# Optimization experiments

Measured on AMD Instinct MI355X. Metric: run time of the kernel, lower is better.

Reference implementation:

```python
import jax, jax.numpy as jnp
import numpy as np

H = 256  # GRU hidden size


def _gru_scan(state, lengths, Wih, Whh, bih, bhh):
    # state: [B, T, D]; run a batched GRU over time, freezing h once t >= lengths[b]
    B, T, D = state.shape
    # precompute input gates for all timesteps: [T, B, 3H]
    gi_all = jnp.einsum('btd,gd->tbg', state, Wih) + bih

    def step(h, inp):
        gi, t = inp
        gh = h @ Whh.T + bhh                       # [B, 3H]
        i_r, i_z, i_n = jnp.split(gi, 3, axis=-1)
        h_r, h_z, h_n = jnp.split(gh, 3, axis=-1)
        r = jax.nn.sigmoid(i_r + h_r)
        z = jax.nn.sigmoid(i_z + h_z)
        n = jnp.tanh(i_n + r * h_n)
        h_new = (1.0 - z) * n + z * h              # torch GRUCell update
        mask = (t < lengths)[:, None]              # ragged: stop updating past length
        return jnp.where(mask, h_new, h), None

    h0 = jnp.zeros((B, H), state.dtype)
    h, _ = jax.lax.scan(step, h0, (gi_all, jnp.arange(T)))
    return h  # [B, H] = hidden after lengths[b] GRU steps


def _mlp(x, w1, b1, w2, b2, w3, b3, w4, b4, wq, bq):
    x = jax.nn.relu(x @ w1.T + b1)
    x = jax.nn.relu(x @ w2.T + b2)
    x = jax.nn.relu(x @ w3.T + b3)
    x = jax.nn.relu(x @ w4.T + b4)
    return x @ wq.T + bq  # [B, 1]


def setup_inputs() -> dict:
    key = jax.random.key(0)
    ks = jax.random.split(key, 40)
    B, T, D, A = 2048, 64, 15, 1
    inp = {}
    inp['state'] = jax.random.normal(ks[0], (B, T, D), jnp.float32)
    inp['action'] = jax.random.normal(ks[1], (B, A), jnp.float32)
    inp['lengths'] = jax.random.randint(ks[2], (B,), 1, T + 1, jnp.int32)
    i = 3
    for t in (1, 2):
        for name, shape, fan in [('Wih', (3 * H, D), D), ('Whh', (3 * H, H), H),
                                 ('bih', (3 * H,), H), ('bhh', (3 * H,), H)]:
            inp[f'g{t}_{name}'] = jax.random.normal(ks[i], shape, jnp.float32) / np.sqrt(fan)
            i += 1
        for name, (o, n) in [('fc1', (1024, H + D + A)), ('fc2', (1024, 1024)),
                             ('fc3', (512, 1024)), ('fc4', (256, 512)), ('q', (1, 256))]:
            inp[f'{name}_{t}_w'] = jax.random.normal(ks[i], (o, n), jnp.float32) / np.sqrt(n)
            i += 1
            inp[f'{name}_{t}_b'] = jax.random.normal(ks[i], (o,), jnp.float32) * 0.01
            i += 1
    return inp


def reference(state, action, lengths,
              g1_Wih, g1_Whh, g1_bih, g1_bhh,
              fc1_1_w, fc1_1_b, fc2_1_w, fc2_1_b, fc3_1_w, fc3_1_b,
              fc4_1_w, fc4_1_b, q_1_w, q_1_b,
              g2_Wih, g2_Whh, g2_bih, g2_bhh,
              fc1_2_w, fc1_2_b, fc2_2_w, fc2_2_b, fc3_2_w, fc3_2_b,
              fc4_2_w, fc4_2_b, q_2_w, q_2_b):
    h1 = _gru_scan(state, lengths, g1_Wih, g1_Whh, g1_bih, g1_bhh)
    h2 = _gru_scan(state, lengths, g2_Wih, g2_Whh, g2_bih, g2_bhh)
    aug = jnp.concatenate([state[:, 0, :], action], axis=-1)  # [B, 16]
    x1 = jnp.concatenate([aug, h1], axis=-1)                  # [B, 272]
    x2 = jnp.concatenate([aug, h2], axis=-1)
    out1 = _mlp(x1, fc1_1_w, fc1_1_b, fc2_1_w, fc2_1_b, fc3_1_w, fc3_1_b,
                fc4_1_w, fc4_1_b, q_1_w, q_1_b)
    out2 = _mlp(x2, fc1_2_w, fc1_2_b, fc2_2_w, fc2_2_b, fc3_2_w, fc3_2_b,
                fc4_2_w, fc4_2_b, q_2_w, q_2_b)
    return (out1, out2)
```

## Files before the change

kernel.cpp:

```cpp
#include <hip/hip_runtime.h>

typedef float  f32x4 __attribute__((ext_vector_type(4)));
typedef short  s16x8 __attribute__((ext_vector_type(8)));
typedef __bf16 b16x8 __attribute__((ext_vector_type(8)));

#define DEV __device__ __forceinline__

DEV unsigned short f2b(float f) {
  unsigned u = __builtin_bit_cast(unsigned, f);
  u = (u + 0x7FFFu + ((u >> 16) & 1u)) >> 16;
  return (unsigned short)u;
}
DEV b16x8 ld8(const unsigned short* p) {
  return __builtin_bit_cast(b16x8, *(const s16x8*)p);
}
DEV float sigm(float x) { return __builtin_amdgcn_rcpf(1.f + __expf(-x)); }
DEV float tanh_fast(float x) {
  float e = __expf(2.f * x);
  return 1.f - 2.f * __builtin_amdgcn_rcpf(e + 1.f);
}
DEV void async16(const unsigned short* g, unsigned short* l) {
  __builtin_amdgcn_global_load_lds(
      (const __attribute__((address_space(1))) unsigned int*)g,
      (__attribute__((address_space(3))) unsigned int*)l, 16, 0, 0);
}
DEV f32x4 mfma_bf16(b16x8 a, b16x8 b, f32x4 c) {
  return __builtin_amdgcn_mfma_f32_16x16x32_bf16(a, b, c, 0, 0, 0);
}

struct PrepArgs {
  const float *whh[2], *wih[2], *bih[2], *bhh[2];
  const float *src[2][4];
  unsigned short *waug[2], *dst[2][4];
  const float *qb[2];
  float *out;
};

__global__ __launch_bounds__(256) void prep_kernel(PrepArgs p) {
  const int job = blockIdx.y;
  const int i0 = blockIdx.x * 256 + threadIdx.x;
  const int stride = gridDim.x * 256;
  if (job < 2) {
    const float* whh = p.whh[job];
    const float* wih = p.wih[job];
    const float* bih = p.bih[job];
    const float* bhh = p.bhh[job];
    unsigned short* dst = p.waug[job];
    for (int idx = i0; idx < 768 * 288; idx += stride) {
      int j = idx / 288, k = idx - j * 288;
      float v = 0.f;
      if (k < 256) {
        int o = k & 31;
        int kk = (k & 0x1E0) + (o >> 1) + ((o & 1) << 4);
        v = whh[j * 256 + kk];
      } else if (k < 271)  v = wih[j * 15 + (k - 256)];
      else if (k == 271)   v = (j < 512) ? (bih[j] + bhh[j]) : bih[j];
      dst[idx] = f2b(v);
    }
  } else if (job < 10) {
    const int jj = job - 2, br = jj >> 2, ly = jj & 3;
    const int rowsA[4] = {1024, 1024, 512, 256};
    const int scA[4]   = {272, 1024, 1024, 512};
    const int dcA[4]   = {288, 1024, 1024, 512};
    const float* src = p.src[br][ly];
    unsigned short* dst = p.dst[br][ly];
    const int sc = scA[ly], dc = dcA[ly], tot = rowsA[ly] * dc;
    for (int idx = i0; idx < tot; idx += stride) {
      int r = idx / dc, c = idx - r * dc;
      float v = (c < sc) ? src[r * sc + c] : 0.f;
      dst[idx] = f2b(v);
    }
  } else {
    for (int idx = i0; idx < 4096; idx += stride)
      p.out[idx] = p.qb[idx >> 11][0];
  }
}

#define GRU_LDS_BYTES 98432
__attribute__((amdgpu_waves_per_eu(2, 2)))
__global__ void __launch_bounds__(512) gru_kernel(
    const float* __restrict__ state, const float* __restrict__ action,
    const int* __restrict__ lengths,
    const unsigned short* __restrict__ waug0, const unsigned short* __restrict__ waug1,
    const float* __restrict__ bhh0, const float* __restrict__ bhh1,
    unsigned short* __restrict__ x0, unsigned short* __restrict__ x1) {
  extern __shared__ char smem[];
  unsigned short* W7   = (unsigned short*)smem;
  unsigned short* SgL  = (unsigned short*)(smem + 49152);
  unsigned*       Hb2  = (unsigned*)(smem + 81920);
  int* lenS = (int*)(smem + 98304);
  int* mlS  = (int*)(smem + 98368);

  const int tid = threadIdx.x;
  const int lane = tid & 63, w = tid >> 6;
  const int l15 = lane & 15, q = lane >> 4;
  const int g = blockIdx.x & 1;
  const int r0 = (blockIdx.x >> 1) * 16;

  const unsigned short* Waug = g ? waug1 : waug0;
  const float* bhh = g ? bhh1 : bhh0;
  unsigned short* xout = g ? x1 : x0;

  for (int i = tid; i < 4096; i += 512) Hb2[i] = 0;
  if (tid < 16) lenS[tid] = lengths[r0 + tid];
  for (int s = tid; s < 64 * 32; s += 512) {
    const int t = s >> 5, L = s & 31;
    const int q2 = L >> 4, r = L & 15;
    const float* sp = state + (size_t)(r0 + r) * 960 + t * 15;
    s16x8 h;
#pragma unroll
    for (int j = 0; j < 8; j++) {
      const int k = q2 * 8 + j;
      float v = (k < 15) ? sp[k] : (k == 15 ? 1.0f : 0.f);
      h[j] = (short)f2b(v);
    }
    *(s16x8*)(SgL + (size_t)s * 8) = h;
  }
  __syncthreads();
  if (tid == 0) {
    int m = 1;
    for (int i = 0; i < 16; i++) m = lenS[i] > m ? lenS[i] : m;
    *mlS = m;
  }

  int c0[6];
  c0[0] = 32 * w;       c0[1] = 32 * w + 16;
  c0[2] = 256 + 32 * w; c0[3] = 256 + 32 * w + 16;
  c0[4] = 512 + 32 * w; c0[5] = 512 + 32 * w + 16;

  b16x8 wres[6][7];
  b16x8 waugf[6];
#pragma unroll
  for (int i = 0; i < 6; i++) {
    const unsigned short* bpi = Waug + (size_t)(c0[i] + l15) * 288 + q * 8;
#pragma unroll
    for (int j = 0; j < 7; j++) wres[i][j] = ld8(bpi + j * 32);
    waugf[i] = ld8(bpi + 256);
    *(s16x8*)(W7 + (size_t)i * 4096 + tid * 8) =
        __builtin_bit_cast(s16x8, ld8(bpi + 7 * 32));
  }
  float bnH[2] = {bhh[c0[4] + l15], bhh[c0[5] + l15]};
  int len4[4];
#pragma unroll
  for (int r = 0; r < 4; r++) len4[r] = lenS[q * 4 + r];

  int aOff[8];
#pragma unroll
  for (int j = 0; j < 8; j++) {
    const int cj = 4 * j + q;
    const int pj = (cj & 24) | ((cj & 7) ^ (l15 & 7));
    aOff[j] = l15 * 128 + pj * 4;
  }
  int wOff[4];
#pragma unroll
  for (int rg = 0; rg < 4; rg++) {
    const int row = q * 4 + rg;
    const int cb = 4 * w + (l15 >> 2);
    const int pw = (cb & 24) | ((cb & 7) ^ (row & 7));
    wOff[rg] = row * 128 + pw * 4 + (l15 & 3);
  }
  __syncthreads();
  const int maxlen = *mlS;

  float hold[2][4] = {{0, 0, 0, 0}, {0, 0, 0, 0}};
  int poff = 0;

  for (int t = 0; t < maxlen; ++t) {
    __syncthreads();

    f32x4 acc[6];
#pragma unroll
    for (int i = 0; i < 6; i++) acc[i] = f32x4{0.f, 0.f, 0.f, 0.f};

    {
      b16x8 a8 = ld8(SgL + t * 256 + ((q & 1) * 16 + l15) * 8);
#pragma unroll
      for (int i = 0; i < 6; i++) acc[i] = mfma_bf16(a8, waugf[i], acc[i]);
    }
    f32x4 giN0 = acc[4], giN1 = acc[5];
    acc[4] = acc[4] + bnH[0];
    acc[5] = acc[5] + bnH[1];

    const unsigned* hb = Hb2 + poff;
#pragma unroll
    for (int j = 0; j < 7; j++) {
      b16x8 a = __builtin_bit_cast(b16x8, *(const uint4*)(hb + aOff[j]));
#pragma unroll
      for (int i = 0; i < 6; i++) acc[i] = mfma_bf16(a, wres[i][j], acc[i]);
    }
    {
      b16x8 a = __builtin_bit_cast(b16x8, *(const uint4*)(hb + aOff[7]));
#pragma unroll
      for (int i = 0; i < 6; i++) {
        b16x8 bw = ld8(W7 + (size_t)i * 4096 + tid * 8);
        acc[i] = mfma_bf16(a, bw, acc[i]);
      }
    }

    unsigned* hbw = Hb2 + (poff ^ 2048);
#pragma unroll
    for (int rg = 0; rg < 4; rg++) {
      const bool live = (t < len4[rg]);
      float r0g = sigm(acc[0][rg]);
      float z0 = sigm(acc[2][rg]);
      float n0 = tanh_fast(giN0[rg] + r0g * (acc[4][rg] - giN0[rg]));
      float h0 = n0 + z0 * (hold[0][rg] - n0);
      h0 = live ? h0 : hold[0][rg];
      hold[0][rg] = h0;
      float r1g = sigm(acc[1][rg]);
      float z1 = sigm(acc[3][rg]);
      float n1 = tanh_fast(giN1[rg] + r1g * (acc[5][rg] - giN1[rg]));
      float h1 = n1 + z1 * (hold[1][rg] - n1);
      h1 = live ? h1 : hold[1][rg];
      hold[1][rg] = h1;
      hbw[wOff[rg]] = (unsigned)f2b(h0) | ((unsigned)f2b(h1) << 16);
    }
    poff ^= 2048;
  }

#pragma unroll
  for (int i = 0; i < 2; i++) {
    const int c = 32 * w + 16 * i + l15;
#pragma unroll
    for (int rg = 0; rg < 4; rg++) {
      const int row = q * 4 + rg;
      xout[(size_t)(r0 + row) * 288 + 16 + c] = f2b(hold[i][rg]);
    }
  }
  {
    const int row = tid >> 5, cc = tid & 31;
    float v; int col;
    if (cc < 15)       { v = state[(size_t)(r0 + row) * 960 + cc]; col = cc; }
    else if (cc == 15) { v = action[r0 + row]; col = 15; }
    else               { v = 0.f; col = 256 + cc; }
    xout[(size_t)(r0 + row) * 288 + col] = f2b(v);
  }
}

template <int BM, int BN>
__global__ __launch_bounds__(256, 2) void gemm_bias_relu(
    const unsigned short* __restrict__ A0, const unsigned short* __restrict__ A1,
    const unsigned short* __restrict__ W0, const unsigned short* __restrict__ W1,
    const float* __restrict__ b0, const float* __restrict__ b1,
    unsigned short* __restrict__ Y0, unsigned short* __restrict__ Y1,
    int N, int K) {
  const unsigned short* A = blockIdx.z ? A1 : A0;
  const unsigned short* W = blockIdx.z ? W1 : W0;
  const float* bias = blockIdx.z ? b1 : b0;
  unsigned short* Y = blockIdx.z ? Y1 : Y0;

  constexpr int MT = BM / 32;
  constexpr int NT = BN / 32;
  const int tid = threadIdx.x;
  const int lane = tid & 63, wid = tid >> 6;
  const int wm = wid >> 1, wn = wid & 1;
  const int l15 = lane & 15, q = lane >> 4;
  const int m0 = blockIdx.x * BM, n0 = blockIdx.y * BN;

  __shared__ unsigned short As[BM * 32];
  __shared__ unsigned short Bs[BN * 32];

  f32x4 acc[MT][NT];
#pragma unroll
  for (int mi = 0; mi < MT; mi++)
#pragma unroll
    for (int ni = 0; ni < NT; ni++) acc[mi][ni] = f32x4{0.f, 0.f, 0.f, 0.f};

  const int srow = tid >> 2, scol = (tid & 3) * 8;

  for (int k0 = 0; k0 < K; k0 += 32) {
#pragma unroll
    for (int g64 = 0; g64 < BM / 64; g64++)
      async16(A + (size_t)(m0 + g64 * 64 + srow) * K + scol + k0,
              &As[g64 * 2048 + tid * 8]);
#pragma unroll
    for (int g64 = 0; g64 < BN / 64; g64++)
      async16(W + (size_t)(n0 + g64 * 64 + srow) * K + scol + k0,
              &Bs[g64 * 2048 + tid * 8]);
    __syncthreads();

    b16x8 af[MT], bf[NT];
#pragma unroll
    for (int mi = 0; mi < MT; mi++)
      af[mi] = ld8(&As[(wm * (BM / 2) + mi * 16 + l15) * 32 + q * 8]);
#pragma unroll
    for (int ni = 0; ni < NT; ni++)
      bf[ni] = ld8(&Bs[(wn * (BN / 2) + ni * 16 + l15) * 32 + q * 8]);
#pragma unroll
    for (int mi = 0; mi < MT; mi++)
#pragma unroll
      for (int ni = 0; ni < NT; ni++)
        acc[mi][ni] = mfma_bf16(af[mi], bf[ni], acc[mi][ni]);
    __syncthreads();
  }

#pragma unroll
  for (int ni = 0; ni < NT; ni++) {
    const int col = n0 + wn * (BN / 2) + ni * 16 + l15;
    const float bv = bias[col];
#pragma unroll
    for (int mi = 0; mi < MT; mi++) {
      const int rbase = m0 + wm * (BM / 2) + mi * 16 + q * 4;
#pragma unroll
      for (int rg = 0; rg < 4; rg++) {
        float v = acc[mi][ni][rg] + bv;
        v = fmaxf(v, 0.f);
        Y[(size_t)(rbase + rg) * N + col] = f2b(v);
      }
    }
  }
}

__global__ __launch_bounds__(256, 2) void fc4q_kernel(
    const unsigned short* __restrict__ A0, const unsigned short* __restrict__ A1,
    const unsigned short* __restrict__ W0, const unsigned short* __restrict__ W1,
    const float* __restrict__ b0, const float* __restrict__ b1,
    const float* __restrict__ qw0, const float* __restrict__ qw1,
    float* __restrict__ out) {
  const unsigned short* A = blockIdx.z ? A1 : A0;
  const unsigned short* W = blockIdx.z ? W1 : W0;
  const float* bias = blockIdx.z ? b1 : b0;
  const float* qw = blockIdx.z ? qw1 : qw0;

  const int tid = threadIdx.x;
  const int lane = tid & 63, wn = tid >> 6;
  const int l15 = lane & 15, q = lane >> 4;
  const int m0 = blockIdx.x * 32;
  const int nbase = blockIdx.y * 128;
  const int K = 512;

  __shared__ unsigned short As[32 * 32];
  __shared__ unsigned short Bs[128 * 32];
  __shared__ float red[32][4];

  f32x4 acc[2][2];
#pragma unroll
  for (int mi = 0; mi < 2; mi++)
#pragma unroll
    for (int ni = 0; ni < 2; ni++) acc[mi][ni] = f32x4{0.f, 0.f, 0.f, 0.f};

  const int srow = tid >> 2, scol = (tid & 3) * 8;
  for (int k0 = 0; k0 < K; k0 += 32) {
    if (tid < 128)
      async16(A + (size_t)(m0 + srow) * K + scol + k0, &As[tid * 8]);
#pragma unroll
    for (int g64 = 0; g64 < 2; g64++)
      async16(W + (size_t)(nbase + g64 * 64 + srow) * K + scol + k0,
              &Bs[g64 * 2048 + tid * 8]);
    __syncthreads();

    b16x8 af[2], bf[2];
#pragma unroll
    for (int mi = 0; mi < 2; mi++)
      af[mi] = ld8(&As[(mi * 16 + l15) * 32 + q * 8]);
#pragma unroll
    for (int ni = 0; ni < 2; ni++)
      bf[ni] = ld8(&Bs[(wn * 32 + ni * 16 + l15) * 32 + q * 8]);
#pragma unroll
    for (int mi = 0; mi < 2; mi++)
#pragma unroll
      for (int ni = 0; ni < 2; ni++)
        acc[mi][ni] = mfma_bf16(af[mi], bf[ni], acc[mi][ni]);
    __syncthreads();
  }

#pragma unroll
  for (int mi = 0; mi < 2; mi++) {
#pragma unroll
    for (int rg = 0; rg < 4; rg++) {
      float s = 0.f;
#pragma unroll
      for (int ni = 0; ni < 2; ni++) {
        const int col = nbase + wn * 32 + ni * 16 + l15;
        float v = fmaxf(acc[mi][ni][rg] + bias[col], 0.f);
        s += v * qw[col];
      }
#pragma unroll
      for (int off = 1; off < 16; off <<= 1) s += __shfl_xor(s, off);
      if (l15 == 0) red[mi * 16 + q * 4 + rg][wn] = s;
    }
  }
  __syncthreads();
  if (tid < 32) {
    float t = red[tid][0] + red[tid][1] + red[tid][2] + red[tid][3];
    atomicAdd(out + (size_t)blockIdx.z * 2048 + m0 + tid, t);
  }
}

extern "C" void kernel_launch(void* const* d_in, const int* in_sizes, int n_in,
                              void* d_out, int out_size, void* d_ws, size_t ws_size,
                              hipStream_t stream) {
  const float* state   = (const float*)d_in[0];
  const float* action  = (const float*)d_in[1];
  const int*   lengths = (const int*)d_in[2];
  const float* g_wih[2] = {(const float*)d_in[3], (const float*)d_in[17]};
  const float* g_whh[2] = {(const float*)d_in[4], (const float*)d_in[18]};
  const float* g_bih[2] = {(const float*)d_in[5], (const float*)d_in[19]};
  const float* g_bhh[2] = {(const float*)d_in[6], (const float*)d_in[20]};
  const float* fcw[2][4] = {
      {(const float*)d_in[7], (const float*)d_in[9], (const float*)d_in[11], (const float*)d_in[13]},
      {(const float*)d_in[21], (const float*)d_in[23], (const float*)d_in[25], (const float*)d_in[27]}};
  const float* fcb[2][4] = {
      {(const float*)d_in[8], (const float*)d_in[10], (const float*)d_in[12], (const float*)d_in[14]},
      {(const float*)d_in[22], (const float*)d_in[24], (const float*)d_in[26], (const float*)d_in[28]}};
  const float* qw[2] = {(const float*)d_in[15], (const float*)d_in[29]};
  const float* qb[2] = {(const float*)d_in[16], (const float*)d_in[30]};
  float* out = (float*)d_out;

  uintptr_t base = (uintptr_t)d_ws;
  auto alloc = [&](size_t bytes) -> unsigned short* {
    void* p = (void*)base;
    base += (bytes + 255) & ~(size_t)255;
    return (unsigned short*)p;
  };
  unsigned short *waug[2], *w1b[2], *w2b[2], *w3b[2], *w4b[2], *xb[2], *yA[2], *yB[2];
  for (int g = 0; g < 2; g++) waug[g] = alloc(768 * 288 * 2);
  for (int g = 0; g < 2; g++) w1b[g] = alloc(1024 * 288 * 2);
  for (int g = 0; g < 2; g++) w2b[g] = alloc(1024 * 1024 * 2);
  for (int g = 0; g < 2; g++) w3b[g] = alloc(512 * 1024 * 2);
  for (int g = 0; g < 2; g++) w4b[g] = alloc(256 * 512 * 2);
  for (int g = 0; g < 2; g++) xb[g] = alloc(2048 * 288 * 2);
  for (int g = 0; g < 2; g++) yA[g] = alloc(2048 * 1024 * 2);
  for (int g = 0; g < 2; g++) yB[g] = alloc(2048 * 1024 * 2);
  (void)ws_size; (void)in_sizes; (void)n_in; (void)out_size;

  PrepArgs pa;
  for (int g = 0; g < 2; g++) {
    pa.whh[g] = g_whh[g]; pa.wih[g] = g_wih[g];
    pa.bih[g] = g_bih[g]; pa.bhh[g] = g_bhh[g];
    pa.waug[g] = waug[g];
    pa.src[g][0] = fcw[g][0]; pa.dst[g][0] = w1b[g];
    pa.src[g][1] = fcw[g][1]; pa.dst[g][1] = w2b[g];
    pa.src[g][2] = fcw[g][2]; pa.dst[g][2] = w3b[g];
    pa.src[g][3] = fcw[g][3]; pa.dst[g][3] = w4b[g];
    pa.qb[g] = qb[g];
  }
  pa.out = out;
  prep_kernel<<<dim3(64, 11), 256, 0, stream>>>(pa);

  (void)hipFuncSetAttribute((const void*)gru_kernel,
                            hipFuncAttributeMaxDynamicSharedMemorySize,
                            GRU_LDS_BYTES);
  gru_kernel<<<dim3(256), dim3(512), GRU_LDS_BYTES, stream>>>(
      state, action, lengths, waug[0], waug[1], g_bhh[0], g_bhh[1], xb[0], xb[1]);

  gemm_bias_relu<64, 128><<<dim3(32, 8, 2), 256, 0, stream>>>(
      xb[0], xb[1], w1b[0], w1b[1], fcb[0][0], fcb[1][0], yA[0], yA[1], 1024, 288);
  gemm_bias_relu<64, 128><<<dim3(32, 8, 2), 256, 0, stream>>>(
      yA[0], yA[1], w2b[0], w2b[1], fcb[0][1], fcb[1][1], yB[0], yB[1], 1024, 1024);
  gemm_bias_relu<64, 64><<<dim3(32, 8, 2), 256, 0, stream>>>(
      yB[0], yB[1], w3b[0], w3b[1], fcb[0][2], fcb[1][2], yA[0], yA[1], 512, 1024);
  fc4q_kernel<<<dim3(64, 2, 2), 256, 0, stream>>>(
      yA[0], yA[1], w4b[0], w4b[1], fcb[0][3], fcb[1][3], qw[0], qw[1], out);
}
```

Baseline: 356.7 us.

## Halve GRU block to 4 waves with 64 columns each; retune MLP GEMM tiles

The GRU recurrence kernel now runs 256 threads instead of 512. Each wave owns 64 hidden columns across all three gates, which doubles the per-wave MFMA work and register-resident weights. The input-projection weights move from registers to LDS, raising the LDS footprint to about 147 KB. The goal is to cut per-step barrier cost and cross-wave sync in the serial time loop, at the price of fewer waves to hide latency and heavy register pressure. Separately, fc1/fc2 use 64x64 tiles with twice as many blocks, and the GEMM launch bounds allow 4 blocks per CU.

```diff
diff --git a/kernel.cpp b/kernel.cpp
--- a/kernel.cpp
+++ b/kernel.cpp
@@ -76,9 +76,9 @@
   }
 }
 
-#define GRU_LDS_BYTES 98432
-__attribute__((amdgpu_waves_per_eu(2, 2)))
-__global__ void __launch_bounds__(512) gru_kernel(
+#define GRU_LDS_BYTES 147584
+__attribute__((amdgpu_waves_per_eu(1, 1)))
+__global__ void __launch_bounds__(256) gru_kernel(
     const float* __restrict__ state, const float* __restrict__ action,
     const int* __restrict__ lengths,
     const unsigned short* __restrict__ waug0, const unsigned short* __restrict__ waug1,
@@ -86,10 +86,11 @@
     unsigned short* __restrict__ x0, unsigned short* __restrict__ x1) {
   extern __shared__ char smem[];
   unsigned short* W7   = (unsigned short*)smem;
-  unsigned short* SgL  = (unsigned short*)(smem + 49152);
-  unsigned*       Hb2  = (unsigned*)(smem + 81920);
-  int* lenS = (int*)(smem + 98304);
-  int* mlS  = (int*)(smem + 98368);
+  unsigned short* WA   = (unsigned short*)(smem + 49152);
+  unsigned short* SgL  = (unsigned short*)(smem + 98304);
+  unsigned*       Hb2  = (unsigned*)(smem + 131072);
+  int* lenS = (int*)(smem + 147456);
+  int* mlS  = (int*)(smem + 147520);
 
   const int tid = threadIdx.x;
   const int lane = tid & 63, w = tid >> 6;
@@ -101,9 +102,9 @@
   const float* bhh = g ? bhh1 : bhh0;
   unsigned short* xout = g ? x1 : x0;
 
-  for (int i = tid; i < 4096; i += 512) Hb2[i] = 0;
+  for (int i = tid; i < 4096; i += 256) Hb2[i] = 0;
   if (tid < 16) lenS[tid] = lengths[r0 + tid];
-  for (int s = tid; s < 64 * 32; s += 512) {
+  for (int s = tid; s < 64 * 32; s += 256) {
     const int t = s >> 5, L = s & 31;
     const int q2 = L >> 4, r = L & 15;
     const float* sp = state + (size_t)(r0 + r) * 960 + t * 15;
@@ -123,112 +124,119 @@
     *mlS = m;
   }
 
-  int c0[6];
-  c0[0] = 32 * w;       c0[1] = 32 * w + 16;
-  c0[2] = 256 + 32 * w; c0[3] = 256 + 32 * w + 16;
-  c0[4] = 512 + 32 * w; c0[5] = 512 + 32 * w + 16;
-
-  b16x8 wres[6][7];
-  b16x8 waugf[6];
-#pragma unroll
-  for (int i = 0; i < 6; i++) {
+  int c0[12];
+#pragma unroll
+  for (int gate = 0; gate < 3; gate++)
+#pragma unroll
+    for (int j = 0; j < 4; j++) c0[gate * 4 + j] = gate * 256 + 64 * w + 16 * j;
+
+  b16x8 wres[12][7];
+#pragma unroll
+  for (int i = 0; i < 12; i++) {
     const unsigned short* bpi = Waug + (size_t)(c0[i] + l15) * 288 + q * 8;
 #pragma unroll
     for (int j = 0; j < 7; j++) wres[i][j] = ld8(bpi + j * 32);
-    waugf[i] = ld8(bpi + 256);
-    *(s16x8*)(W7 + (size_t)i * 4096 + tid * 8) =
+    *(s16x8*)(W7 + ((size_t)i * 256 + tid) * 8) =
         __builtin_bit_cast(s16x8, ld8(bpi + 7 * 32));
-  }
-  float bnH[2] = {bhh[c0[4] + l15], bhh[c0[5] + l15]};
+    *(s16x8*)(WA + ((size_t)i * 256 + tid) * 8) =
+        __builtin_bit_cast(s16x8, ld8(bpi + 256));
+  }
+  float bnH[4];
+#pragma unroll
+  for (int j = 0; j < 4; j++) bnH[j] = bhh[c0[8 + j] + l15];
   int len4[4];
 #pragma unroll
   for (int r = 0; r < 4; r++) len4[r] = lenS[q * 4 + r];
 
   int aOff[8];
 #pragma unroll
-  for (int j = 0; j < 8; j++) {
-    const int cj = 4 * j + q;
-    const int pj = (cj & 24) | ((cj & 7) ^ (l15 & 7));
-    aOff[j] = l15 * 128 + pj * 4;
-  }
-  int wOff[4];
-#pragma unroll
-  for (int rg = 0; rg < 4; rg++) {
-    const int row = q * 4 + rg;
-    const int cb = 4 * w + (l15 >> 2);
-    const int pw = (cb & 24) | ((cb & 7) ^ (row & 7));
-    wOff[rg] = row * 128 + pw * 4 + (l15 & 3);
-  }
+  for (int k = 0; k < 8; k++) {
+    const int ck = 4 * k + q;
+    const int pk = (ck & 24) | ((ck & 7) ^ (l15 & 7));
+    aOff[k] = l15 * 128 + pk * 4;
+  }
+  int wOff[2][4];
+#pragma unroll
+  for (int p = 0; p < 2; p++)
+#pragma unroll
+    for (int rg = 0; rg < 4; rg++) {
+      const int row = q * 4 + rg;
+      const int cb = 8 * w + 4 * p + (l15 >> 2);
+      const int pw = (cb & 24) | ((cb & 7) ^ (row & 7));
+      wOff[p][rg] = row * 128 + pw * 4 + (l15 & 3);
+    }
   __syncthreads();
   const int maxlen = *mlS;
 
-  float hold[2][4] = {{0, 0, 0, 0}, {0, 0, 0, 0}};
+  float hold[4][4] = {{0,0,0,0},{0,0,0,0},{0,0,0,0},{0,0,0,0}};
   int poff = 0;
 
   for (int t = 0; t < maxlen; ++t) {
     __syncthreads();
 
-    f32x4 acc[6];
-#pragma unroll
-    for (int i = 0; i < 6; i++) acc[i] = f32x4{0.f, 0.f, 0.f, 0.f};
+    f32x4 acc[12];
+#pragma unroll
+    for (int i = 0; i < 12; i++) acc[i] = f32x4{0.f, 0.f, 0.f, 0.f};
 
     {
       b16x8 a8 = ld8(SgL + t * 256 + ((q & 1) * 16 + l15) * 8);
 #pragma unroll
-      for (int i = 0; i < 6; i++) acc[i] = mfma_bf16(a8, waugf[i], acc[i]);
-    }
-    f32x4 giN0 = acc[4], giN1 = acc[5];
-    acc[4] = acc[4] + bnH[0];
-    acc[5] = acc[5] + bnH[1];
+      for (int i = 0; i < 12; i++) {
+        b16x8 bw = ld8(WA + ((size_t)i * 256 + tid) * 8);
+        acc[i] = mfma_bf16(a8, bw, acc[i]);
+      }
+    }
+    f32x4 giN[4];
+#pragma unroll
+    for (int j = 0; j < 4; j++) { giN[j] = acc[8 + j]; acc[8 + j] = acc[8 + j] + bnH[j]; }
 
     const unsigned* hb = Hb2 + poff;
 #pragma unroll
-    for (int j = 0; j < 7; j++) {
-      b16x8 a = __builtin_bit_cast(b16x8, *(const uint4*)(hb + aOff[j]));
-#pragma unroll
-      for (int i = 0; i < 6; i++) acc[i] = mfma_bf16(a, wres[i][j], acc[i]);
+    for (int k = 0; k < 7; k++) {
+      b16x8 a = __builtin_bit_cast(b16x8, *(const uint4*)(hb + aOff[k]));
+#pragma unroll
+      for (int i = 0; i < 12; i++) acc[i] = mfma_bf16(a, wres[i][k], acc[i]);
     }
     {
       b16x8 a = __builtin_bit_cast(b16x8, *(const uint4*)(hb + aOff[7]));
 #pragma unroll
-      for (int i = 0; i < 6; i++) {
-        b16x8 bw = ld8(W7 + (size_t)i * 4096 + tid * 8);
+      for (int i = 0; i < 12; i++) {
+        b16x8 bw = ld8(W7 + ((size_t)i * 256 + tid) * 8);
         acc[i] = mfma_bf16(a, bw, acc[i]);
       }
     }
 
     unsigned* hbw = Hb2 + (poff ^ 2048);
 #pragma unroll
-    for (int rg = 0; rg < 4; rg++) {
-      const bool live = (t < len4[rg]);
-      float r0g = sigm(acc[0][rg]);
-      float z0 = sigm(acc[2][rg]);
-      float n0 = tanh_fast(giN0[rg] + r0g * (acc[4][rg] - giN0[rg]));
-      float h0 = n0 + z0 * (hold[0][rg] - n0);
-      h0 = live ? h0 : hold[0][rg];
-      hold[0][rg] = h0;
-      float r1g = sigm(acc[1][rg]);
-      float z1 = sigm(acc[3][rg]);
-      float n1 = tanh_fast(giN1[rg] + r1g * (acc[5][rg] - giN1[rg]));
-      float h1 = n1 + z1 * (hold[1][rg] - n1);
-      h1 = live ? h1 : hold[1][rg];
-      hold[1][rg] = h1;
-      hbw[wOff[rg]] = (unsigned)f2b(h0) | ((unsigned)f2b(h1) << 16);
-    }
+    for (int j = 0; j < 4; j++)
+#pragma unroll
+      for (int rg = 0; rg < 4; rg++) {
+        const bool live = (t < len4[rg]);
+        float r = sigm(acc[j][rg]);
+        float z = sigm(acc[4 + j][rg]);
+        float n = tanh_fast(giN[j][rg] + r * (acc[8 + j][rg] - giN[j][rg]));
+        float h = n + z * (hold[j][rg] - n);
+        h = live ? h : hold[j][rg];
+        hold[j][rg] = h;
+      }
+#pragma unroll
+    for (int p = 0; p < 2; p++)
+#pragma unroll
+      for (int rg = 0; rg < 4; rg++)
+        hbw[wOff[p][rg]] = (unsigned)f2b(hold[2 * p][rg]) |
+                           ((unsigned)f2b(hold[2 * p + 1][rg]) << 16);
     poff ^= 2048;
   }
 
 #pragma unroll
-  for (int i = 0; i < 2; i++) {
-    const int c = 32 * w + 16 * i + l15;
+  for (int j = 0; j < 4; j++)
 #pragma unroll
     for (int rg = 0; rg < 4; rg++) {
       const int row = q * 4 + rg;
-      xout[(size_t)(r0 + row) * 288 + 16 + c] = f2b(hold[i][rg]);
-    }
-  }
-  {
-    const int row = tid >> 5, cc = tid & 31;
+      xout[(size_t)(r0 + row) * 288 + 16 + c0[j] + l15] = f2b(hold[j][rg]);
+    }
+  for (int s = tid; s < 512; s += 256) {
+    const int row = s >> 5, cc = s & 31;
     float v; int col;
     if (cc < 15)       { v = state[(size_t)(r0 + row) * 960 + cc]; col = cc; }
     else if (cc == 15) { v = action[r0 + row]; col = 15; }
@@ -238,7 +246,7 @@
 }
 
 template <int BM, int BN>
-__global__ __launch_bounds__(256, 2) void gemm_bias_relu(
+__global__ __launch_bounds__(256, 4) void gemm_bias_relu(
     const unsigned short* __restrict__ A0, const unsigned short* __restrict__ A1,
     const unsigned short* __restrict__ W0, const unsigned short* __restrict__ W1,
     const float* __restrict__ b0, const float* __restrict__ b1,
@@ -311,7 +319,7 @@
   }
 }
 
-__global__ __launch_bounds__(256, 2) void fc4q_kernel(
+__global__ __launch_bounds__(256, 4) void fc4q_kernel(
     const unsigned short* __restrict__ A0, const unsigned short* __restrict__ A1,
     const unsigned short* __restrict__ W0, const unsigned short* __restrict__ W1,
     const float* __restrict__ b0, const float* __restrict__ b1,
@@ -441,12 +449,12 @@
   (void)hipFuncSetAttribute((const void*)gru_kernel,
                             hipFuncAttributeMaxDynamicSharedMemorySize,
                             GRU_LDS_BYTES);
-  gru_kernel<<<dim3(256), dim3(512), GRU_LDS_BYTES, stream>>>(
+  gru_kernel<<<dim3(256), dim3(256), GRU_LDS_BYTES, stream>>>(
       state, action, lengths, waug[0], waug[1], g_bhh[0], g_bhh[1], xb[0], xb[1]);
 
-  gemm_bias_relu<64, 128><<<dim3(32, 8, 2), 256, 0, stream>>>(
+  gemm_bias_relu<64, 64><<<dim3(32, 16, 2), 256, 0, stream>>>(
       xb[0], xb[1], w1b[0], w1b[1], fcb[0][0], fcb[1][0], yA[0], yA[1], 1024, 288);
-  gemm_bias_relu<64, 128><<<dim3(32, 8, 2), 256, 0, stream>>>(
+  gemm_bias_relu<64, 64><<<dim3(32, 16, 2), 256, 0, stream>>>(
       yA[0], yA[1], w2b[0], w2b[1], fcb[0][1], fcb[1][1], yB[0], yB[1], 1024, 1024);
   gemm_bias_relu<64, 64><<<dim3(32, 8, 2), 256, 0, stream>>>(
       yB[0], yB[1], w3b[0], w3b[1], fcb[0][2], fcb[1][2], yA[0], yA[1], 512, 1024);
```

After: 356.2 us. About the same (-0.1%).
